# Performance work log

Hardware: AMD Instinct MI355X
Metric: run time of the kernel (lower is better)

## Reference

```python
import jax, jax.numpy as jnp
import numpy as np

HEAD = 12
EPS = float(np.finfo(np.float32).eps)  # torch RMSNorm default eps = finfo(dtype).eps


def _rmsnorm(v, g):
    # v: [B,H,T,dh], g: [dh]
    ms = jnp.mean(v * v, axis=-1, keepdims=True)
    return v * jax.lax.rsqrt(ms + EPS) * g


def setup_inputs() -> dict:
    key = jax.random.key(0)
    k1, k2, k3, k4, k5 = jax.random.split(key, 5)
    B, T, C = 2, 2048, 768
    x = jax.random.normal(k1, (B, T, C), dtype=jnp.float32)
    # nn.Linear(feats, feats, bias=False) weight: [out, in]
    W = jax.random.normal(k2, (C, C), dtype=jnp.float32) * (1.0 / np.sqrt(C))
    dh = C // HEAD
    g1 = jnp.ones((dh,), dtype=jnp.float32)
    g2 = jnp.ones((dh,), dtype=jnp.float32)
    g3 = jnp.ones((dh,), dtype=jnp.float32)
    return {"x": x, "W": W, "g1": g1, "g2": g2, "g3": g3}


def reference(x, W, g1, g2, g3):
    B, T, C = x.shape
    dh = C // HEAD
    sqrt_d = np.sqrt(dh).astype(np.float32)
    # qkv projection (shared weights): w = x @ W.T -> [B,H,T,dh]
    w = (x @ W.T).reshape(B, T, HEAD, dh).transpose(0, 2, 1, 3)
    q = _rmsnorm(w, g1)
    k = _rmsnorm(w, g2)
    v = _rmsnorm(w, g3)
    # full T x T score matrix (intentionally materialized, as in the module)
    att = jnp.einsum('bhif,bhjf->bhij', q, k) / sqrt_d
    a = jax.nn.softmax(att, axis=-1) + jax.nn.softmax(att, axis=-2)  # bisoftmax
    y = jnp.einsum('bhij,bhjf->bihf', a, v).reshape(B, T, C)
    # F.linear(y, W.t()) == y @ W
    return y @ W
```

## Files before the change

### kernel.cpp

```cpp
#include <hip/hip_runtime.h>

constexpr int T_SEQ = 2048;
constexpr int CDIM  = 768;
constexpr int HEADS = 12;
constexpr int DH    = 64;
constexpr int BATCH = 2;
constexpr int BH_TOT = BATCH * HEADS;
constexpr int NROWS  = BATCH * T_SEQ;
constexpr float RMS_EPS = 1.1920929e-07f;
constexpr float QSCALE = 0.18033688011112042f;


typedef __attribute__((ext_vector_type(8))) short bf16x8;
typedef __attribute__((ext_vector_type(4))) float f32x4;
typedef __attribute__((ext_vector_type(4))) unsigned int u32x4;

__device__ __forceinline__ unsigned short f2bf(float f) {
    union { float f; unsigned int u; } v; v.f = f;
    unsigned int u = v.u;
    unsigned int r = (u + 0x7fffu + ((u >> 16) & 1u)) >> 16;
    return (unsigned short)r;
}
__device__ __forceinline__ float b2f(unsigned short h) {
    union { unsigned int u; float f; } v; v.u = ((unsigned int)h) << 16;
    return v.f;
}
__device__ __forceinline__ unsigned int cvt_pk_bf16(float lo, float hi) {
    unsigned int r;
    asm("v_cvt_pk_bf16_f32 %0, %1, %2" : "=v"(r) : "v"(lo), "v"(hi));
    return r;
}
__device__ __forceinline__ float fast_exp2(float x) {
    float r;
    asm("v_exp_f32 %0, %1" : "=v"(r) : "v"(x));
    return r;
}
__device__ __forceinline__ float fast_rcp(float x) {
    return __builtin_amdgcn_rcpf(x);
}
__device__ __forceinline__ void gld_lds16(const void* g, void* l) {
    __builtin_amdgcn_global_load_lds(
        (const __attribute__((address_space(1))) void*)g,
        (__attribute__((address_space(3))) void*)l, 16, 0, 0);
}
__device__ __forceinline__ void stageLin(const unsigned short* g, unsigned short* l, int tid) {
#pragma unroll
    for (int p = 0; p < 4; ++p) {
        int d = (p * 256 + tid) * 16;
        gld_lds16((const char*)g + d, (char*)l + d);
    }
}
__device__ __forceinline__ void stage8k(const unsigned short* g, unsigned short* l, int tid) {
#pragma unroll
    for (int p = 0; p < 2; ++p) {
        int d = (p * 256 + tid) * 16;
        gld_lds16((const char*)g + d, (char*)l + d);
    }
}

__global__ __launch_bounds__(256) void prep_kernel(
    const float* __restrict__ x, const float* __restrict__ W,
    unsigned short* __restrict__ xh,
    unsigned short* __restrict__ Wh, unsigned short* __restrict__ WTh)
{
    const size_t NC = (size_t)NROWS * CDIM;
    const size_t WSZ = (size_t)CDIM * CDIM;
    size_t stride = (size_t)gridDim.x * blockDim.x;
    for (size_t i = (size_t)blockIdx.x * blockDim.x + threadIdx.x; i < NC; i += stride)
        xh[i] = f2bf(x[i]);
    for (size_t i = (size_t)blockIdx.x * blockDim.x + threadIdx.x; i < WSZ; i += stride) {
        unsigned short h = f2bf(W[i]);
        Wh[i] = h;
        size_t k = i / CDIM, c = i % CDIM;
        WTh[c * CDIM + k] = h;
    }
}

__global__ __launch_bounds__(256) void gemm64_nt(
    const unsigned short* __restrict__ A, const unsigned short* __restrict__ B,
    float* __restrict__ C, int M, int N, int K, int ldc)
{
    __shared__ unsigned short sA[2][64 * 64], sB[2][64 * 64];
    const int tid = threadIdx.x;
    const int lane = tid & 63;
    const int wv = tid >> 6;
    const int wr = wv >> 1, wc = wv & 1;
    const int li = lane & 15, g = lane >> 4;

    const int nbx = N / 64;
    const int wgid = blockIdx.x;
    const int xcd = wgid & 7;
    const int idx = wgid >> 3;
    const int perx = (M / 64) / 8;
    const int my = xcd * perx + idx / nbx;
    const int nx = idx % nbx;
    const int M0 = my * 64, N0 = nx * 64;

    f32x4 acc[2][2];
#pragma unroll
    for (int i = 0; i < 2; ++i)
#pragma unroll
        for (int j = 0; j < 2; ++j) acc[i][j] = (f32x4)0.0f;

#pragma unroll
    for (int p = 0; p < 2; ++p) {
        int dd = tid * 16 + p * 4096;
        int row = dd >> 7;
        int cb = (dd & 127) ^ ((row & 7) << 4);
        gld_lds16((const char*)A + ((size_t)(M0 + row) * K) * 2 + cb, (char*)sA[0] + dd);
        gld_lds16((const char*)B + ((size_t)(N0 + row) * K) * 2 + cb, (char*)sB[0] + dd);
    }

    int buf = 0;
    for (int k0 = 0; k0 < K; k0 += 64) {
        __syncthreads();
        if (k0 + 64 < K) {
#pragma unroll
            for (int p = 0; p < 2; ++p) {
                int dd = tid * 16 + p * 4096;
                int row = dd >> 7;
                int cb = (dd & 127) ^ ((row & 7) << 4);
                gld_lds16((const char*)A + ((size_t)(M0 + row) * K + k0 + 64) * 2 + cb,
                          (char*)sA[buf ^ 1] + dd);
                gld_lds16((const char*)B + ((size_t)(N0 + row) * K + k0 + 64) * 2 + cb,
                          (char*)sB[buf ^ 1] + dd);
            }
        }
#pragma unroll
        for (int ks = 0; ks < 2; ++ks) {
            const int ko = ks * 32 + g * 8;
            bf16x8 a[2], b[2];
#pragma unroll
            for (int mi = 0; mi < 2; ++mi) {
                int r = wr * 32 + mi * 16 + li;
                a[mi] = *(const bf16x8*)((char*)sA[buf] + ((r * 128 + ko * 2) ^ ((r & 7) << 4)));
            }
#pragma unroll
            for (int ni = 0; ni < 2; ++ni) {
                int r = wc * 32 + ni * 16 + li;
                b[ni] = *(const bf16x8*)((char*)sB[buf] + ((r * 128 + ko * 2) ^ ((r & 7) << 4)));
            }
#pragma unroll
            for (int mi = 0; mi < 2; ++mi)
#pragma unroll
                for (int ni = 0; ni < 2; ++ni)
                    acc[mi][ni] = __builtin_amdgcn_mfma_f32_16x16x32_bf16(a[mi], b[ni], acc[mi][ni], 0, 0, 0);
        }
        buf ^= 1;
    }
#pragma unroll
    for (int mi = 0; mi < 2; ++mi)
#pragma unroll
        for (int ni = 0; ni < 2; ++ni)
#pragma unroll
            for (int r = 0; r < 4; ++r) {
                int row = M0 + wr * 32 + mi * 16 + g * 4 + r;
                int col = N0 + wc * 32 + ni * 16 + li;
                C[(size_t)row * ldc + col] = acc[mi][ni][r];
            }
}

__global__ __launch_bounds__(256) void rmsqkv_kernel(
    const float* __restrict__ wbuf,
    const float* __restrict__ g1, const float* __restrict__ g2, const float* __restrict__ g3,
    unsigned short* __restrict__ qbf, unsigned short* __restrict__ kbf,
    unsigned short* __restrict__ vb)
{
    const int d = threadIdx.x & 63;
    const int wv = threadIdx.x >> 6;
    const int ridx = blockIdx.x * 4 + wv;
    const int bt = ridx / HEADS;
    const int h = ridx % HEADS;
    const int b = bt >> 11, t = bt & (T_SEQ - 1);

    float v = wbuf[(size_t)bt * CDIM + h * DH + d];
    float ss = v * v;
#pragma unroll
    for (int m = 32; m; m >>= 1) ss += __shfl_xor(ss, m);
    float r = rsqrtf(ss * (1.0f / 64.0f) + RMS_EPS);
    float wn = v * r;

    const int bh = b * HEADS + h;
    size_t fidx = (size_t)bh * (T_SEQ * DH)
                + (size_t)(t >> 7) * 8192
                + (size_t)((((t & 127) >> 4) * 2 + (d >> 5)) * 512
                           + ((d >> 3) & 3) * 128 + (t & 15) * 8 + (d & 7));
    qbf[fidx] = f2bf(wn * g1[d] * QSCALE);
    kbf[fidx] = f2bf(wn * g2[d]);
    vb[((size_t)bh * T_SEQ + t) * DH + d] = f2bf(wn * g3[d]);
}

__global__ __launch_bounds__(256) void vtrans_kernel(
    const unsigned short* __restrict__ vb, unsigned short* __restrict__ vTf)
{
    __shared__ unsigned short raw[128 * 72];
    const int bh = blockIdx.y, jt = blockIdx.x;
    const int tid = threadIdx.x;
    const unsigned short* src = &vb[((size_t)bh * T_SEQ + jt * 128) * DH];
#pragma unroll
    for (int p = 0; p < 4; ++p) {
        int i16 = p * 256 + tid;
        int r = i16 >> 3, c8 = i16 & 7;
        *(u32x4*)&raw[r * 72 + c8 * 8] = *(const u32x4*)&src[r * 64 + c8 * 8];
    }
    __syncthreads();
    unsigned short* dst = &vTf[(size_t)bh * (T_SEQ * DH) + (size_t)jt * 8192];
#pragma unroll
    for (int p = 0; p < 4; ++p) {
        int c = p * 256 + tid;
        int li = c & 15, g = (c >> 4) & 3, ni = (c >> 6) & 3, ks2 = c >> 8;
        int f = ni * 16 + li;
        int j0 = ks2 * 32 + g * 8;
        u32x4 out;
#pragma unroll
        for (int k = 0; k < 4; ++k) {
            unsigned int lo = raw[(j0 + 2 * k) * 72 + f];
            unsigned int hi = raw[(j0 + 2 * k + 1) * 72 + f];
            out[k] = lo | (hi << 16);
        }
        *(u32x4*)&dst[c * 8] = out;
    }
}

__global__ __launch_bounds__(256) void sums_kernel(
    const unsigned short* __restrict__ qbf, const unsigned short* __restrict__ kbf,
    float* __restrict__ rowsum, float* __restrict__ colsum)
{
    __shared__ unsigned short sQ[2][8192];
    const int tid = threadIdx.x;
    const int lane = tid & 63;
    const int w = tid >> 6;
    const int li = lane & 15;
    const int g = lane >> 4;

    const int wgid = blockIdx.x;
    const int xcd = wgid & 7;
    const int idx = wgid >> 3;
    const int bh = xcd * 3 + (idx >> 6);
    const int w2 = idx & 63;
    const int jx = w2 & 15;
    const int iy = w2 >> 4;
    const int J0 = jx * 128;

    const unsigned short* ktile = kbf + (size_t)bh * (T_SEQ * DH) + (size_t)jx * 8192;
    bf16x8 kf[2][2];
#pragma unroll
    for (int jb = 0; jb < 2; ++jb)
#pragma unroll
        for (int ks = 0; ks < 2; ++ks)
            kf[jb][ks] = *(const bf16x8*)&ktile[(size_t)((((w * 2 + jb) * 2 + ks) * 64 + lane) * 8)];

    const unsigned short* qbase = qbf + (size_t)bh * (T_SEQ * DH) + (size_t)(iy * 4) * 8192;
    stageLin(qbase, sQ[0], tid);
    __syncthreads();

    float csum[2][4];
#pragma unroll
    for (int jb = 0; jb < 2; ++jb)
#pragma unroll
        for (int r = 0; r < 4; ++r) csum[jb][r] = 0.0f;

    for (int it = 0; it < 4; ++it) {
        const int I0 = iy * 512 + it * 128;
        if (it + 1 < 4)
            stageLin(qbase + (size_t)(it + 1) * 8192, sQ[(it + 1) & 1], tid);
        const unsigned short* q = sQ[it & 1];

#pragma unroll
        for (int half = 0; half < 2; ++half) {
            f32x4 acc[2][4];
#pragma unroll
            for (int jb = 0; jb < 2; ++jb)
#pragma unroll
                for (int ib = 0; ib < 4; ++ib) acc[jb][ib] = (f32x4)0.0f;
#pragma unroll
            for (int ks = 0; ks < 2; ++ks) {
#pragma unroll
                for (int ib = 0; ib < 4; ++ib) {
                    bf16x8 qf = *(const bf16x8*)&q[(((half * 4 + ib) * 2 + ks) * 64 + lane) * 8];
#pragma unroll
                    for (int jb = 0; jb < 2; ++jb)
                        acc[jb][ib] = __builtin_amdgcn_mfma_f32_16x16x32_bf16(kf[jb][ks], qf, acc[jb][ib], 0, 0, 0);
                }
            }
#pragma unroll
            for (int ib = 0; ib < 4; ++ib) {
                float rp = 0.0f;
#pragma unroll
                for (int jb = 0; jb < 2; ++jb)
#pragma unroll
                    for (int r = 0; r < 4; ++r) {
                        float e = fast_exp2(acc[jb][ib][r]);
                        csum[jb][r] += e;
                        rp += e;
                    }
                rp += __shfl_xor(rp, 16);
                rp += __shfl_xor(rp, 32);
                if (g == 0)
                    atomicAdd(&rowsum[(size_t)bh * T_SEQ + I0 + half * 64 + ib * 16 + li], rp);
            }
        }
        __syncthreads();
    }
#pragma unroll
    for (int jb = 0; jb < 2; ++jb)
#pragma unroll
        for (int r = 0; r < 4; ++r) {
            float c = csum[jb][r];
            c += __shfl_xor(c, 1); c += __shfl_xor(c, 2);
            c += __shfl_xor(c, 4); c += __shfl_xor(c, 8);
            if (li == 0)
                atomicAdd(&colsum[(size_t)bh * T_SEQ + J0 + w * 32 + jb * 16 + g * 4 + r], c);
        }
}

__global__ __launch_bounds__(256) void inv_kernel(float* __restrict__ s, int n4)
{
    int i = blockIdx.x * 256 + threadIdx.x;
    if (i < n4) {
        f32x4 v = ((f32x4*)s)[i];
        v[0] = fast_rcp(v[0]); v[1] = fast_rcp(v[1]);
        v[2] = fast_rcp(v[2]); v[3] = fast_rcp(v[3]);
        ((f32x4*)s)[i] = v;
    }
}

__global__ __launch_bounds__(256) void fused_pv_kernel(
    const unsigned short* __restrict__ qbf, const unsigned short* __restrict__ kbf,
    const unsigned short* __restrict__ vTf,
    const float* __restrict__ rowinv, const float* __restrict__ colinv,
    unsigned short* __restrict__ yh)
{
    __shared__ unsigned short sK[4096];
    __shared__ unsigned short sV[4096];
    __shared__ unsigned short sP[4096];

    const int tid = threadIdx.x;
    const int lane = tid & 63;
    const int w = tid >> 6;
    const int li = lane & 15;
    const int g = lane >> 4;

    const int wgid = blockIdx.x;
    const int xcd = wgid & 7;
    const int idx = wgid >> 3;
    const int bh = xcd * 3 + (idx >> 5);
    const int it = idx & 31;
    const int I0 = it * 64;
    constexpr int NT = T_SEQ / 64;

    const int rbq = ((I0 & 127) >> 4) + w;
    const unsigned short* qtile = qbf + (size_t)bh * (T_SEQ * DH) + (size_t)(I0 >> 7) * 8192;
    bf16x8 qf[2];
#pragma unroll
    for (int ks = 0; ks < 2; ++ks)
        qf[ks] = *(const bf16x8*)&qtile[(size_t)(((rbq * 2 + ks) * 64 + lane) * 8)];
    const float rv = rowinv[bh * T_SEQ + I0 + w * 16 + li];

    char* const sPw = (char*)sP + w * 2048;

    f32x4 accy[4];
#pragma unroll
    for (int i = 0; i < 4; ++i) accy[i] = (f32x4)0.0f;

    const size_t bhbase = (size_t)bh * (T_SEQ * DH);
    const unsigned short* kt0 = kbf + bhbase;
    const unsigned short* vt0 = vTf + bhbase;

    stage8k(kt0, sK, tid);
    stage8k(vt0, sV, tid);
    __syncthreads();

    for (int jt = 0; jt < NT; ++jt) {
        f32x4 accs[4];
#pragma unroll
        for (int jb = 0; jb < 4; ++jb) accs[jb] = (f32x4)0.0f;
#pragma unroll
        for (int ks = 0; ks < 2; ++ks) {
#pragma unroll
            for (int jb = 0; jb < 4; ++jb) {
                bf16x8 kfr = *(const bf16x8*)&sK[((jb * 2 + ks) * 64 + lane) * 8];
                accs[jb] = __builtin_amdgcn_mfma_f32_16x16x32_bf16(kfr, qf[ks], accs[jb], 0, 0, 0);
            }
        }

#pragma unroll
        for (int jb = 0; jb < 4; ++jb) {
            f32x4 cv = *(const f32x4*)&colinv[(size_t)bh * T_SEQ + jt * 64 + jb * 16 + g * 4];
            float p0 = fast_exp2(accs[jb][0]) * (rv + cv[0]);
            float p1 = fast_exp2(accs[jb][1]) * (rv + cv[1]);
            float p2 = fast_exp2(accs[jb][2]) * (rv + cv[2]);
            float p3 = fast_exp2(accs[jb][3]) * (rv + cv[3]);
            uint2 pw;
            pw.x = cvt_pk_bf16(p0, p1);
            pw.y = cvt_pk_bf16(p2, p3);
            int off = ((jb >> 1) * 4 + (jb & 1) * 2 + (g >> 1)) * 256 + li * 16 + (g & 1) * 8;
            *(uint2*)(sPw + off) = pw;
        }

        __syncthreads();
        if (jt + 1 < NT)
            stage8k(kt0 + (size_t)(jt + 1) * 4096, sK, tid);

#pragma unroll
        for (int ks2 = 0; ks2 < 2; ++ks2) {
            bf16x8 pf = *(const bf16x8*)(sPw + ((ks2 * 4 + g) * 256 + li * 16));
#pragma unroll
            for (int ni = 0; ni < 4; ++ni) {
                bf16x8 vf = *(const bf16x8*)&sV[(ks2 * 256 + ni * 64 + lane) * 8];
                accy[ni] = __builtin_amdgcn_mfma_f32_16x16x32_bf16(pf, vf, accy[ni], 0, 0, 0);
            }
        }

        __syncthreads();
        if (jt + 1 < NT)
            stage8k(vt0 + (size_t)(jt + 1) * 4096, sV, tid);
    }

    const int b_ = bh / HEADS, h = bh % HEADS;
#pragma unroll
    for (int ni = 0; ni < 4; ++ni)
#pragma unroll
        for (int r = 0; r < 4; ++r) {
            int i = I0 + w * 16 + g * 4 + r;
            int col = h * DH + ni * 16 + li;
            yh[((size_t)b_ * T_SEQ + i) * CDIM + col] = f2bf(accy[ni][r]);
        }
}

extern "C" void kernel_launch(void* const* d_in, const int* in_sizes, int n_in,
                              void* d_out, int out_size, void* d_ws, size_t ws_size,
                              hipStream_t stream)
{
    const float* x  = (const float*)d_in[0];
    const float* W  = (const float*)d_in[1];
    const float* g1 = (const float*)d_in[2];
    const float* g2 = (const float*)d_in[3];
    const float* g3 = (const float*)d_in[4];
    float* out = (float*)d_out;

    char* p = (char*)d_ws;
    auto alloc = [&](size_t bytes) -> void* {
        void* r = (void*)p;
        p += (bytes + 255) & ~(size_t)255;
        return r;
    };
    const size_t NC  = (size_t)NROWS * CDIM;
    const size_t WSZ = (size_t)CDIM * CDIM;
    const size_t QSZ = (size_t)BH_TOT * T_SEQ * DH;

    unsigned short* xh   = (unsigned short*)alloc(NC * 2);
    unsigned short* Wh   = (unsigned short*)alloc(WSZ * 2);
    unsigned short* WTh  = (unsigned short*)alloc(WSZ * 2);
    float*          wbuf = (float*)alloc(NC * 4);
    unsigned short* qbf  = (unsigned short*)alloc(QSZ * 2);
    unsigned short* kbf  = (unsigned short*)alloc(QSZ * 2);
    unsigned short* vb   = (unsigned short*)alloc(QSZ * 2);
    unsigned short* vTf  = (unsigned short*)alloc(QSZ * 2);
    unsigned short* yh   = (unsigned short*)alloc(NC * 2);
    float* rowsum = (float*)alloc((size_t)BH_TOT * T_SEQ * 4 * 2);
    float* colsum = rowsum + (size_t)BH_TOT * T_SEQ;

    prep_kernel<<<2048, 256, 0, stream>>>(x, W, xh, Wh, WTh);
    gemm64_nt<<<(NROWS / 64) * (CDIM / 64), 256, 0, stream>>>(
        xh, Wh, wbuf, NROWS, CDIM, CDIM, CDIM);
    rmsqkv_kernel<<<(NROWS * HEADS) / 4, 256, 0, stream>>>(
        wbuf, g1, g2, g3, qbf, kbf, vb);
    vtrans_kernel<<<dim3(T_SEQ / 128, BH_TOT), 256, 0, stream>>>(vb, vTf);

    hipMemsetAsync(rowsum, 0, (size_t)BH_TOT * T_SEQ * 4 * 2, stream);
    sums_kernel<<<(T_SEQ / 128) * 4 * BH_TOT, 256, 0, stream>>>(
        qbf, kbf, rowsum, colsum);
    {
        int n4 = BH_TOT * T_SEQ * 2 / 4;
        inv_kernel<<<(n4 + 255) / 256, 256, 0, stream>>>(rowsum, n4);
    }

    fused_pv_kernel<<<(T_SEQ / 64) * BH_TOT, 256, 0, stream>>>(
        qbf, kbf, vTf, rowsum, colsum, yh);

    gemm64_nt<<<(NROWS / 64) * (CDIM / 64), 256, 0, stream>>>(
        yh, WTh, out, NROWS, CDIM, CDIM, CDIM);
}
```

Before: 131.8 us.

## Split fused PV kernel over key dimension and reduce partials

Splits the key/value sequence range of the fused attention-PV kernel into two halves, doubling the workgroup count from 768 to 1536 so more CUs stay busy and each block loops over half as many tiles. Each half writes fp32 partial outputs to a new workspace buffer, and a new reduce kernel sums the two halves and converts to bf16 in the head-interleaved layout. In exchange it adds an extra launch plus about 25 MB of fp32 partial-result traffic. Q-fragment loads and the prologue are also repeated per split.

```diff
diff --git a/kernel.cpp b/kernel.cpp
--- a/kernel.cpp
+++ b/kernel.cpp
@@ -7,6 +7,7 @@
 constexpr int BATCH = 2;
 constexpr int BH_TOT = BATCH * HEADS;
 constexpr int NROWS  = BATCH * T_SEQ;
+constexpr int JS     = 2;
 constexpr float RMS_EPS = 1.1920929e-07f;
 constexpr float QSCALE = 0.18033688011112042f;
 
@@ -329,7 +330,7 @@
     const unsigned short* __restrict__ qbf, const unsigned short* __restrict__ kbf,
     const unsigned short* __restrict__ vTf,
     const float* __restrict__ rowinv, const float* __restrict__ colinv,
-    unsigned short* __restrict__ yh)
+    float* __restrict__ ypart)
 {
     __shared__ unsigned short sK[4096];
     __shared__ unsigned short sV[4096];
@@ -344,10 +345,13 @@
     const int wgid = blockIdx.x;
     const int xcd = wgid & 7;
     const int idx = wgid >> 3;
-    const int bh = xcd * 3 + (idx >> 5);
-    const int it = idx & 31;
+    const int grp = xcd * 6 + (idx >> 5);
+    const int it  = idx & 31;
+    const int bh = grp >> 1;
+    const int jc = grp & 1;
     const int I0 = it * 64;
-    constexpr int NT = T_SEQ / 64;
+    const int J0 = jc * (T_SEQ / JS);
+    constexpr int NT = T_SEQ / JS / 64;
 
     const int rbq = ((I0 & 127) >> 4) + w;
     const unsigned short* qtile = qbf + (size_t)bh * (T_SEQ * DH) + (size_t)(I0 >> 7) * 8192;
@@ -364,8 +368,8 @@
     for (int i = 0; i < 4; ++i) accy[i] = (f32x4)0.0f;
 
     const size_t bhbase = (size_t)bh * (T_SEQ * DH);
-    const unsigned short* kt0 = kbf + bhbase;
-    const unsigned short* vt0 = vTf + bhbase;
+    const unsigned short* kt0 = kbf + bhbase + (size_t)(J0 >> 6) * 4096;
+    const unsigned short* vt0 = vTf + bhbase + (size_t)(J0 >> 6) * 4096;
 
     stage8k(kt0, sK, tid);
     stage8k(vt0, sV, tid);
@@ -386,7 +390,7 @@
 
 #pragma unroll
         for (int jb = 0; jb < 4; ++jb) {
-            f32x4 cv = *(const f32x4*)&colinv[(size_t)bh * T_SEQ + jt * 64 + jb * 16 + g * 4];
+            f32x4 cv = *(const f32x4*)&colinv[(size_t)bh * T_SEQ + J0 + jt * 64 + jb * 16 + g * 4];
             float p0 = fast_exp2(accs[jb][0]) * (rv + cv[0]);
             float p1 = fast_exp2(accs[jb][1]) * (rv + cv[1]);
             float p2 = fast_exp2(accs[jb][2]) * (rv + cv[2]);
@@ -417,15 +421,34 @@
             stage8k(vt0 + (size_t)(jt + 1) * 4096, sV, tid);
     }
 
-    const int b_ = bh / HEADS, h = bh % HEADS;
 #pragma unroll
     for (int ni = 0; ni < 4; ++ni)
 #pragma unroll
         for (int r = 0; r < 4; ++r) {
             int i = I0 + w * 16 + g * 4 + r;
-            int col = h * DH + ni * 16 + li;
-            yh[((size_t)b_ * T_SEQ + i) * CDIM + col] = f2bf(accy[ni][r]);
-        }
+            int f = ni * 16 + li;
+            ypart[(((size_t)jc * BH_TOT + bh) * T_SEQ + i) * DH + f] = accy[ni][r];
+        }
+}
+
+__global__ __launch_bounds__(256) void reduce_kernel(
+    const float* __restrict__ ypart, unsigned short* __restrict__ yh)
+{
+    const size_t STR = (size_t)BH_TOT * T_SEQ * DH;
+    size_t idx = (size_t)blockIdx.x * 256 + threadIdx.x;
+    if (idx >= STR / 4) return;
+    f32x4 a = *(const f32x4*)&ypart[idx * 4];
+    f32x4 b = *(const f32x4*)&ypart[STR + idx * 4];
+    int e = (int)(idx * 4);
+    int f = e & 63;
+    int rrow = e >> 6;
+    int t = rrow & (T_SEQ - 1);
+    int bh = rrow >> 11;
+    int b_ = bh / HEADS, h = bh % HEADS;
+    size_t o = ((size_t)b_ * T_SEQ + t) * CDIM + h * DH + f;
+#pragma unroll
+    for (int q = 0; q < 4; ++q)
+        yh[o + q] = f2bf(a[q] + b[q]);
 }
 
 extern "C" void kernel_launch(void* const* d_in, const int* in_sizes, int n_in,
@@ -458,6 +481,7 @@
     unsigned short* vb   = (unsigned short*)alloc(QSZ * 2);
     unsigned short* vTf  = (unsigned short*)alloc(QSZ * 2);
     unsigned short* yh   = (unsigned short*)alloc(NC * 2);
+    float* ypart  = (float*)alloc((size_t)JS * QSZ * 4);
     float* rowsum = (float*)alloc((size_t)BH_TOT * T_SEQ * 4 * 2);
     float* colsum = rowsum + (size_t)BH_TOT * T_SEQ;
 
@@ -476,8 +500,12 @@
         inv_kernel<<<(n4 + 255) / 256, 256, 0, stream>>>(rowsum, n4);
     }
 
-    fused_pv_kernel<<<(T_SEQ / 64) * BH_TOT, 256, 0, stream>>>(
-        qbf, kbf, vTf, rowsum, colsum, yh);
+    fused_pv_kernel<<<(T_SEQ / 64) * JS * BH_TOT, 256, 0, stream>>>(
+        qbf, kbf, vTf, rowsum, colsum, ypart);
+    {
+        size_t n4 = (size_t)BH_TOT * T_SEQ * DH / 4;
+        reduce_kernel<<<(unsigned)((n4 + 255) / 256), 256, 0, stream>>>(ypart, yh);
+    }
 
     gemm64_nt<<<(NROWS / 64) * (CDIM / 64), 256, 0, stream>>>(
         yh, WTh, out, NROWS, CDIM, CDIM, CDIM);
```

After: 138.6 us. 1.05x slower.
